# Performance work log

Measured on AMD Instinct MI355X. Metric: run time of the kernel, lower is better.

Reference implementation:

```python
import jax, jax.numpy as jnp
import numpy as np
import itertools

B, T, C, H = 2, 2048, 1024, 8
HD = C // H  # head_dim = 128


def _head_dirs():
    # 8 trigrams = vertices of cube {-1,+1}^3, L2-normalized (norm sqrt(3))
    signs = [-1.0, 1.0]
    tri = np.array(list(itertools.product(signs, repeat=3)), dtype=np.float32)
    tri = tri / np.linalg.norm(tri, axis=1, keepdims=True)
    return jnp.asarray(tri[:H])  # [H, 3]


def setup_inputs() -> dict:
    key = jax.random.key(0)
    ks = jax.random.split(key, 5)
    w = lambda k, sh: jax.random.normal(k, sh, dtype=jnp.float32) * 0.02
    return {
        "x": jax.random.normal(ks[0], (B, T, C), dtype=jnp.float32),
        "Wq": w(ks[1], (H * 3, C)),
        "Wk": w(ks[2], (H * 3, C)),
        "Wv": w(ks[3], (C, C)),
        "Wo": w(ks[4], (C, C)),
        "scale": jnp.asarray(1.0 / np.sqrt(3.0), dtype=jnp.float32),
    }


def reference(x, Wq, Wk, Wv, Wo, scale):
    Bb, Tt, Cc = x.shape
    dirs = _head_dirs()  # [H, 3] constant buffer
    # tiny 3-dim per-head Q/K projections
    q3 = (x @ Wq.T).reshape(Bb, Tt, H, 3).transpose(0, 2, 1, 3)  # [B,H,T,3]
    k3 = (x @ Wk.T).reshape(Bb, Tt, H, 3).transpose(0, 2, 1, 3)  # [B,H,T,3]
    v = (x @ Wv.T).reshape(Bb, Tt, H, HD).transpose(0, 2, 1, 3)  # [B,H,T,HD]
    # projections of q/k onto each head's trigram direction
    q_on_dir = jnp.einsum('bhtd,hd->bht', q3, dirs)  # [B,H,T]
    k_on_dir = jnp.einsum('bhtd,hd->bht', k3, dirs)  # [B,H,T]
    # scores = scaled 3-dim dot product + geometric outer-product bias
    scores = jnp.einsum('bhtd,bhsd->bhts', q3, k3) * scale \
        + q_on_dir[..., :, None] * k_on_dir[..., None, :]  # [B,H,T,T]
    causal = jnp.tril(jnp.ones((Tt, Tt), dtype=bool))
    scores = jnp.where(causal, scores, -jnp.inf)
    attn = jax.nn.softmax(scores, axis=-1)
    out = jnp.einsum('bhts,bhsd->bhtd', attn, v)  # [B,H,T,HD]
    out = out.transpose(0, 2, 1, 3).reshape(Bb, Tt, Cc)
    return out @ Wo.T
```

## Files before the change

kernel.cpp:

```cpp
#include <hip/hip_runtime.h>
#include <hip/hip_bf16.h>

#define B_  2
#define T_  2048
#define C_  1024
#define H_  8
#define HD_ 128
#define M_  (B_*T_)

typedef short  bf16x8 __attribute__((ext_vector_type(8)));
typedef float  f32x4  __attribute__((ext_vector_type(4)));
typedef unsigned short u16x8 __attribute__((ext_vector_type(8)));

typedef const __attribute__((address_space(1))) void* gas_ptr;
typedef __attribute__((address_space(3))) void*       las_ptr;

#define L2E_ 1.4426950408889634f

static __device__ __forceinline__ unsigned short f2bf(float f) {
    unsigned int u = __float_as_uint(f);
    u += 0x7fffu + ((u >> 16) & 1u);
    return (unsigned short)(u >> 16);
}
static __device__ __forceinline__ float bf2f(unsigned short u) {
    return __uint_as_float(((unsigned int)u) << 16);
}
static __device__ __forceinline__ float exp2_fast(float x) {
#if __has_builtin(__builtin_amdgcn_exp2f)
    return __builtin_amdgcn_exp2f(x);
#else
    return exp2f(x);
#endif
}

__global__ __launch_bounds__(256) void k_convert_w(const float* __restrict__ Wv,
                                                   const float* __restrict__ Wo,
                                                   unsigned short* __restrict__ wvbf,
                                                   unsigned short* __restrict__ wobf) {
    int i = blockIdx.x * 256 + threadIdx.x;
    const float* src; unsigned short* dst; int off;
    if (i < 262144) { src = Wv; dst = wvbf; off = i; }
    else            { src = Wo; dst = wobf; off = i - 262144; }
    float4 v = reinterpret_cast<const float4*>(src)[off];
    ushort4 o;
    o.x = f2bf(v.x); o.y = f2bf(v.y); o.z = f2bf(v.z); o.w = f2bf(v.w);
    reinterpret_cast<ushort4*>(dst)[off] = o;
}

__global__ __launch_bounds__(256) void k_proj_qk(const float* __restrict__ x,
                                                 const float* __restrict__ Wq,
                                                 const float* __restrict__ Wk,
                                                 const float* __restrict__ scale_p,
                                                 float* __restrict__ qt,
                                                 float* __restrict__ kt,
                                                 unsigned short* __restrict__ xbf) {
    __shared__ __align__(16) float wl[48][260];
    __shared__ __align__(16) float xl[16][260];
    __shared__ float res[16][48];
    const int tid  = threadIdx.x;
    const int row0 = blockIdx.x << 4;
    const int r    = tid >> 4, sub = tid & 15;
    float a0 = 0.f, a1 = 0.f, a2 = 0.f;

    for (int ch = 0; ch < 4; ++ch) {
        const int k0 = ch * 256;
        #pragma unroll
        for (int i = 0; i < 12; ++i) {
            int fi = i * 256 + tid;
            int wr = fi >> 6, wc = (fi & 63) * 4;
            const float* src = (wr < 24) ? (Wq + (size_t)wr * C_) : (Wk + (size_t)(wr - 24) * C_);
            *reinterpret_cast<float4*>(&wl[wr][wc]) = *reinterpret_cast<const float4*>(src + k0 + wc);
        }
        #pragma unroll
        for (int i = 0; i < 4; ++i) {
            int fi = i * 256 + tid;
            int xr = fi >> 6, xc = (fi & 63) * 4;
            size_t goff = (size_t)(row0 + xr) * C_ + k0 + xc;
            float4 xv = *reinterpret_cast<const float4*>(x + goff);
            *reinterpret_cast<float4*>(&xl[xr][xc]) = xv;
            ushort4 o;
            o.x = f2bf(xv.x); o.y = f2bf(xv.y); o.z = f2bf(xv.z); o.w = f2bf(xv.w);
            *reinterpret_cast<ushort4*>(xbf + goff) = o;
        }
        __syncthreads();
        const int oc = sub * 3;
        #pragma unroll 4
        for (int k = 0; k < 256; k += 4) {
            float4 xv = *reinterpret_cast<const float4*>(&xl[r][k]);
            float4 w0 = *reinterpret_cast<const float4*>(&wl[oc + 0][k]);
            float4 w1 = *reinterpret_cast<const float4*>(&wl[oc + 1][k]);
            float4 w2 = *reinterpret_cast<const float4*>(&wl[oc + 2][k]);
            a0 += xv.x * w0.x + xv.y * w0.y + xv.z * w0.z + xv.w * w0.w;
            a1 += xv.x * w1.x + xv.y * w1.y + xv.z * w1.z + xv.w * w1.w;
            a2 += xv.x * w2.x + xv.y * w2.y + xv.z * w2.z + xv.w * w2.w;
        }
        __syncthreads();
    }
    res[r][sub * 3 + 0] = a0;
    res[r][sub * 3 + 1] = a1;
    res[r][sub * 3 + 2] = a2;
    __syncthreads();

    {
        const int rr = tid >> 4, s2 = tid & 15;
        const int isK = s2 >> 3, h = s2 & 7;
        const float r3 = 0.57735026918962576f;
        float d0 = (h & 4) ? r3 : -r3;
        float d1 = (h & 2) ? r3 : -r3;
        float d2 = (h & 1) ? r3 : -r3;
        const float* v3 = &res[rr][isK * 24 + h * 3];
        float a = v3[0], b = v3[1], c = v3[2];
        float ond = a * d0 + b * d1 + c * d2;
        float sc = scale_p[0];
        float4 ov = isK ? make_float4(a, b, c, ond)
                        : make_float4(a * sc * L2E_, b * sc * L2E_, c * sc * L2E_, ond * L2E_);
        float* dst = isK ? kt : qt;
        int grow = row0 + rr;
        int b_ = grow >> 11, t_idx = grow & (T_ - 1);
        reinterpret_cast<float4*>(dst)[(size_t)(b_ * H_ + h) * T_ + t_idx] = ov;
    }
}

template <int MODE>
__global__ __launch_bounds__(256) void k_gemm128x64(const unsigned short* __restrict__ A,
                                                    const unsigned short* __restrict__ Bw,
                                                    void* __restrict__ Cout,
                                                    int Mdim, int Ndim, int Kdim) {
    __shared__ __align__(16) unsigned short lds_a[8][128][8];
    __shared__ __align__(16) unsigned short lds_b[8][64][8];
    const int tid = threadIdx.x;
    const int nbn = Ndim >> 6;
    const int bm = (blockIdx.x / nbn) << 7;
    const int bn = (blockIdx.x % nbn) << 6;
    const int w = tid >> 6, l = tid & 63;
    const int wm = (w >> 1) << 6, wn = (w & 1) << 5;
    const int lh = l & 15, lq = l >> 4;

    f32x4 acc[4][2];
    #pragma unroll
    for (int i = 0; i < 4; ++i)
        #pragma unroll
        for (int j = 0; j < 2; ++j)
            acc[i][j] = (f32x4){0.f, 0.f, 0.f, 0.f};

    for (int k0 = 0; k0 < Kdim; k0 += 64) {
        #pragma unroll
        for (int p = 0; p < 4; ++p) {
            int flat = p * 256 + tid;
            int kq = flat >> 7, row = flat & 127;
            __builtin_amdgcn_global_load_lds((gas_ptr)(A + (size_t)(bm + row) * Kdim + k0 + kq * 8),
                (las_ptr)(&lds_a[0][0][0] + (size_t)flat * 8), 16, 0, 0);
        }
        #pragma unroll
        for (int p = 0; p < 2; ++p) {
            int flat = p * 256 + tid;
            int kq = flat >> 6, row = flat & 63;
            __builtin_amdgcn_global_load_lds((gas_ptr)(Bw + (size_t)(bn + row) * Kdim + k0 + kq * 8),
                (las_ptr)(&lds_b[0][0][0] + (size_t)flat * 8), 16, 0, 0);
        }
        __syncthreads();

        #pragma unroll
        for (int kk = 0; kk < 2; ++kk) {
            bf16x8 af[4], bfr[2];
            #pragma unroll
            for (int f = 0; f < 4; ++f)
                af[f] = *reinterpret_cast<const bf16x8*>(&lds_a[lq + 4 * kk][wm + f * 16 + lh][0]);
            #pragma unroll
            for (int f = 0; f < 2; ++f)
                bfr[f] = *reinterpret_cast<const bf16x8*>(&lds_b[lq + 4 * kk][wn + f * 16 + lh][0]);
            #pragma unroll
            for (int i = 0; i < 4; ++i)
                #pragma unroll
                for (int j = 0; j < 2; ++j)
                    acc[i][j] = __builtin_amdgcn_mfma_f32_16x16x32_bf16(af[i], bfr[j], acc[i][j], 0, 0, 0);
        }
        __syncthreads();
    }

    if constexpr (MODE == 0) {
        float* Cf = (float*)Cout;
        #pragma unroll
        for (int i = 0; i < 4; ++i) {
            int rbase = bm + wm + i * 16 + lq * 4;
            #pragma unroll
            for (int j = 0; j < 2; ++j) {
                int cidx = bn + wn + j * 16 + lh;
                #pragma unroll
                for (int r = 0; r < 4; ++r)
                    Cf[(size_t)(rbase + r) * Ndim + cidx] = acc[i][j][r];
            }
        }
    } else {
        __shared__ unsigned short ldsT[128][72];
        #pragma unroll
        for (int i = 0; i < 4; ++i)
            #pragma unroll
            for (int j = 0; j < 2; ++j)
                #pragma unroll
                for (int r = 0; r < 4; ++r)
                    ldsT[wm + i * 16 + lq * 4 + r][wn + j * 16 + lh] = f2bf(acc[i][j][r]);
        __syncthreads();
        unsigned short* vt_out = (unsigned short*)Cout;
        int c = tid & 63, part = tid >> 6;
        int b = bm >> 11, t0 = bm & (T_ - 1);
        unsigned short* dst = vt_out + ((size_t)b * C_ + bn + c) * T_ + t0 + part * 32;
        #pragma unroll
        for (int jj = 0; jj < 4; ++jj) {
            u16x8 v;
            #pragma unroll
            for (int k = 0; k < 8; ++k) v[k] = ldsT[part * 32 + jj * 8 + k][c];
            *reinterpret_cast<u16x8*>(dst + jj * 8) = v;
        }
    }
}

__global__ __launch_bounds__(256) void k_attn64(
        const float4* __restrict__ qt, const float4* __restrict__ kt,
        const unsigned short* __restrict__ vt,
        unsigned short* __restrict__ mpart,
        float2* __restrict__ mlbuf,
        int nsp, int lg2nsp) {
    __shared__ __align__(16) unsigned short lv[2][8192];
    __shared__ __align__(16) float4 lk[2][64];
    const int tid = threadIdx.x;
    const int w = tid >> 6, l = tid & 63;
    const int lh = l & 15, lg = l >> 4;
    const int bid = blockIdx.x;
    const int qb = 31 - (bid >> (4 + lg2nsp));
    const int sp = (bid >> 4) & (nsp - 1);
    const int bh = bid & 15;
    const int q0 = qb << 6;
    const int qrow = q0 + 4 * lh + w;
    const int nt = qb + 1;

    const float4* qtb = qt + (size_t)bh * T_;
    const float4* ktb = kt + (size_t)bh * T_;
    const unsigned short* vtb = vt + (size_t)bh * HD_ * T_;

    const unsigned short* vsrc[4];
    #pragma unroll
    for (int i = 0; i < 4; ++i) {
        int f = i * 256 + tid;
        vsrc[i] = vtb + (size_t)((((f >> 6) & 7) * 16) + (f & 15)) * T_
                      + ((f >> 9) << 5) + ((f >> 4) & 3) * 8;
    }

#define STAGE(ST, BUF) do {                                                    \
    int s0_ = (ST) << 6;                                                       \
    __builtin_amdgcn_global_load_lds((gas_ptr)(vsrc[0] + s0_),                 \
        (las_ptr)(&lv[BUF][0] + (size_t)(0 * 256 + tid) * 8), 16, 0, 0);       \
    __builtin_amdgcn_global_load_lds((gas_ptr)(vsrc[1] + s0_),                 \
        (las_ptr)(&lv[BUF][0] + (size_t)(1 * 256 + tid) * 8), 16, 0, 0);       \
    __builtin_amdgcn_global_load_lds((gas_ptr)(vsrc[2] + s0_),                 \
        (las_ptr)(&lv[BUF][0] + (size_t)(2 * 256 + tid) * 8), 16, 0, 0);       \
    __builtin_amdgcn_global_load_lds((gas_ptr)(vsrc[3] + s0_),                 \
        (las_ptr)(&lv[BUF][0] + (size_t)(3 * 256 + tid) * 8), 16, 0, 0);       \
    __builtin_amdgcn_global_load_lds((gas_ptr)(ktb + s0_ + l),                 \
        (las_ptr)(&lk[BUF][0]), 16, 0, 0);                                     \
} while (0)

    const float4 q4 = qtb[qrow];
    f32x4 acc[8];
    #pragma unroll
    for (int n = 0; n < 8; ++n) acc[n] = (f32x4){0.f, 0.f, 0.f, 0.f};
    float m = -1e30f, lsum = 0.f;

    if (sp < nt) STAGE(sp, 0);
    __syncthreads();

    int buf = 0;
    for (int st = sp; st < nt; st += nsp) {
        if (st + nsp < nt) STAGE(st + nsp, buf ^ 1);

        const int s0 = st << 6;
        const int c0 = s0 + lg * 8;
        const int c1 = s0 + 32 + lg * 8;

        float p[16];
        float mt = -1e30f;
        #pragma unroll
        for (int jj = 0; jj < 8; ++jj) {
            float4 k4 = lk[buf][lg * 8 + jj];
            float sc = fmaf(q4.x, k4.x, fmaf(q4.y, k4.y, fmaf(q4.z, k4.z, q4.w * k4.w)));
            sc = (c0 + jj > qrow) ? -1e30f : sc;
            p[jj] = sc;
            mt = fmaxf(mt, sc);
        }
        #pragma unroll
        for (int jj = 0; jj < 8; ++jj) {
            float4 k4 = lk[buf][32 + lg * 8 + jj];
            float sc = fmaf(q4.x, k4.x, fmaf(q4.y, k4.y, fmaf(q4.z, k4.z, q4.w * k4.w)));
            sc = (c1 + jj > qrow) ? -1e30f : sc;
            p[8 + jj] = sc;
            mt = fmaxf(mt, sc);
        }
        mt = fmaxf(mt, __shfl_xor(mt, 16));
        mt = fmaxf(mt, __shfl_xor(mt, 32));
        if (__any(mt > m + 8.f)) {
            float mnew = fmaxf(m, mt);
            float corr = exp2_fast(m - mnew);
            m = mnew;
            lsum *= corr;
            float cc0 = __shfl(corr, 4 * lg + 0);
            float cc1 = __shfl(corr, 4 * lg + 1);
            float cc2 = __shfl(corr, 4 * lg + 2);
            float cc3 = __shfl(corr, 4 * lg + 3);
            #pragma unroll
            for (int n = 0; n < 8; ++n) {
                acc[n][0] *= cc0; acc[n][1] *= cc1; acc[n][2] *= cc2; acc[n][3] *= cc3;
            }
        }
        float ps = 0.f;
        #pragma unroll
        for (int jj = 0; jj < 8; ++jj) {
            float e = exp2_fast(p[jj] - m);
            e = (c0 + jj > qrow) ? 0.f : e;
            p[jj] = e;
            ps += e;
        }
        #pragma unroll
        for (int jj = 0; jj < 8; ++jj) {
            float e = exp2_fast(p[8 + jj] - m);
            e = (c1 + jj > qrow) ? 0.f : e;
            p[8 + jj] = e;
            ps += e;
        }
        ps += __shfl_xor(ps, 16);
        ps += __shfl_xor(ps, 32);
        lsum += ps;

        bf16x8 pa0, pa1;
        #pragma unroll
        for (int jj = 0; jj < 8; ++jj) { pa0[jj] = (short)f2bf(p[jj]); pa1[jj] = (short)f2bf(p[8 + jj]); }

        #pragma unroll
        for (int n = 0; n < 8; ++n) {
            bf16x8 vf = *reinterpret_cast<const bf16x8*>(&lv[buf][(size_t)(n * 64 + lg * 16 + lh) * 8]);
            acc[n] = __builtin_amdgcn_mfma_f32_16x16x32_bf16(pa0, vf, acc[n], 0, 0, 0);
        }
        #pragma unroll
        for (int n = 0; n < 8; ++n) {
            bf16x8 vf = *reinterpret_cast<const bf16x8*>(&lv[buf][(size_t)(512 + n * 64 + lg * 16 + lh) * 8]);
            acc[n] = __builtin_amdgcn_mfma_f32_16x16x32_bf16(pa1, vf, acc[n], 0, 0, 0);
        }

        __syncthreads();
        buf ^= 1;
    }
#undef STAGE

    unsigned short* mp = mpart + (size_t)(sp * 16 + bh) * T_ * HD_;
    #pragma unroll
    for (int n = 0; n < 8; ++n) {
        #pragma unroll
        for (int r = 0; r < 4; ++r) {
            int row = q0 + 16 * lg + 4 * r + w;
            mp[(size_t)row * HD_ + n * 16 + lh] = f2bf(acc[n][r]);
        }
    }
    if (lg == 0)
        mlbuf[(size_t)(sp * 16 + bh) * T_ + qrow] = make_float2(m, lsum);
}

__global__ __launch_bounds__(256) void k_combine(const unsigned short* __restrict__ mpart,
                                                 const float2* __restrict__ mlbuf,
                                                 unsigned short* __restrict__ attnbf,
                                                 int nsp) {
    int idx = blockIdx.x * 256 + threadIdx.x;
    int bh = idx >> 16;
    int rem = idx & 65535;
    int t = rem >> 5, d0 = (rem & 31) * 4;
    float mg = -1e30f, den = 0.f;
    float ax = 0.f, ay = 0.f, az = 0.f, aw = 0.f;
    for (int s = 0; s < nsp; ++s) {
        float2 ml = mlbuf[(size_t)(s * 16 + bh) * T_ + t];
        ushort4 a = *reinterpret_cast<const ushort4*>(
            mpart + ((size_t)(s * 16 + bh) * T_ + t) * HD_ + d0);
        float mn = fmaxf(mg, ml.x);
        float cOld = exp2_fast(mg - mn);
        float cNew = exp2_fast(ml.x - mn);
        den = den * cOld + ml.y * cNew;
        ax = ax * cOld + bf2f(a.x) * cNew;
        ay = ay * cOld + bf2f(a.y) * cNew;
        az = az * cOld + bf2f(a.z) * cNew;
        aw = aw * cOld + bf2f(a.w) * cNew;
        mg = mn;
    }
    float inv = 1.f / den;
    int b = bh >> 3, h = bh & 7;
    ushort4 o;
    o.x = f2bf(ax * inv); o.y = f2bf(ay * inv);
    o.z = f2bf(az * inv); o.w = f2bf(aw * inv);
    *reinterpret_cast<ushort4*>(attnbf + ((size_t)(b * T_ + t) * C_ + h * HD_ + d0)) = o;
}

extern "C" void kernel_launch(void* const* d_in, const int* in_sizes, int n_in,
                              void* d_out, int out_size, void* d_ws, size_t ws_size,
                              hipStream_t stream) {
    const float* x     = (const float*)d_in[0];
    const float* Wq    = (const float*)d_in[1];
    const float* Wk    = (const float*)d_in[2];
    const float* Wv    = (const float*)d_in[3];
    const float* Wo    = (const float*)d_in[4];
    const float* scale = (const float*)d_in[5];
    float* out = (float*)d_out;

    const int nsp    = (ws_size >= 46137344) ? 4 : 2;
    const int lg2nsp = (nsp == 4) ? 2 : 1;

    char* ws = (char*)d_ws;
    size_t o = (size_t)nsp * 8388608;
    unsigned short* mpart  = (unsigned short*)(ws);
    unsigned short* xbf    = (unsigned short*)(ws);
    unsigned short* wvbf   = (unsigned short*)(ws + 8388608);
    float*          qt     = (float*)(ws + o);
    float*          kt     = (float*)(ws + o + 524288);
    unsigned short* vt     = (unsigned short*)(ws + o + 1048576);
    unsigned short* attnbf = (unsigned short*)(ws + o + 1048576);
    unsigned short* wobf   = (unsigned short*)(ws + o + 9437184);
    float2*         mlbuf  = (float2*)(ws + o + 11534336);

    k_convert_w<<<2048, 256, 0, stream>>>(Wv, Wo, wvbf, wobf);

    k_proj_qk<<<M_ / 16, 256, 0, stream>>>(x, Wq, Wk, scale, qt, kt, xbf);

    k_gemm128x64<2><<<(M_ / 128) * (C_ / 64), 256, 0, stream>>>(xbf, wvbf, (void*)vt, M_, C_, C_);

    k_attn64<<<32 * nsp * 16, 256, 0, stream>>>(
        reinterpret_cast<const float4*>(qt), reinterpret_cast<const float4*>(kt), vt,
        mpart, mlbuf, nsp, lg2nsp);

    k_combine<<<4096, 256, 0, stream>>>(mpart, mlbuf, attnbf, nsp);

    k_gemm128x64<0><<<(M_ / 128) * (C_ / 64), 256, 0, stream>>>(attnbf, wobf, (void*)out, M_, C_, C_);
}
```

Measured before the change: 134.5 us.

## Pair causal query blocks per workgroup to share K/V tiles

Each attention workgroup now handles two query blocks, a short one (qa) and its mirrored long one (31-qa). The K/V tiles staged into LDS are reused by both, which halves the grid and evens out the causal triangle's work across blocks. Causal masking is applied only on the diagonal tile, and bf16 packing now uses a perm instruction. The cost is doubled accumulator registers (two sets of 8 f32x4), which may lower occupancy, and with nsp>1 the guard `sp < nt` was dropped, so some splits may stage tiles they never use.

```diff
diff --git a/kernel.cpp b/kernel.cpp
--- a/kernel.cpp
+++ b/kernel.cpp
@@ -11,6 +11,7 @@
 typedef short  bf16x8 __attribute__((ext_vector_type(8)));
 typedef float  f32x4  __attribute__((ext_vector_type(4)));
 typedef unsigned short u16x8 __attribute__((ext_vector_type(8)));
+typedef unsigned int   u32x4 __attribute__((ext_vector_type(4)));
 
 typedef const __attribute__((address_space(1))) void* gas_ptr;
 typedef __attribute__((address_space(3))) void*       las_ptr;
@@ -21,6 +22,10 @@
     unsigned int u = __float_as_uint(f);
     u += 0x7fffu + ((u >> 16) & 1u);
     return (unsigned short)(u >> 16);
+}
+static __device__ __forceinline__ unsigned int rne_u32(float f) {
+    unsigned int u = __float_as_uint(f);
+    return u + 0x7fffu + ((u >> 16) & 1u);
 }
 static __device__ __forceinline__ float bf2f(unsigned short u) {
     return __uint_as_float(((unsigned int)u) << 16);
@@ -215,7 +220,7 @@
     }
 }
 
-__global__ __launch_bounds__(256) void k_attn64(
+__global__ __launch_bounds__(256) void k_attn_pair64(
         const float4* __restrict__ qt, const float4* __restrict__ kt,
         const unsigned short* __restrict__ vt,
         unsigned short* __restrict__ mpart,
@@ -227,12 +232,15 @@
     const int w = tid >> 6, l = tid & 63;
     const int lh = l & 15, lg = l >> 4;
     const int bid = blockIdx.x;
-    const int qb = 31 - (bid >> (4 + lg2nsp));
-    const int sp = (bid >> 4) & (nsp - 1);
-    const int bh = bid & 15;
-    const int q0 = qb << 6;
-    const int qrow = q0 + 4 * lh + w;
-    const int nt = qb + 1;
+    const int pr  = bid >> (4 + lg2nsp);
+    const int sp  = (bid >> 4) & (nsp - 1);
+    const int bh  = bid & 15;
+    const int qa  = pr;
+    const int qbg = 31 - pr;
+    const int q0a = qa << 6, q0b = qbg << 6;
+    const int qrowA = q0a + 4 * lh + w;
+    const int qrowB = q0b + 4 * lh + w;
+    const int nt = qbg + 1;
 
     const float4* qtb = qt + (size_t)bh * T_;
     const float4* ktb = kt + (size_t)bh * T_;
@@ -260,13 +268,105 @@
         (las_ptr)(&lk[BUF][0]), 16, 0, 0);                                     \
 } while (0)
 
-    const float4 q4 = qtb[qrow];
-    f32x4 acc[8];
+#define TILE_GROUP(Q4, MM, LS, ACC, EDGE, QROW) do {                           \
+    float p[16];                                                               \
+    if (!(EDGE)) {                                                             \
+        _Pragma("unroll")                                                      \
+        for (int jj = 0; jj < 8; ++jj) {                                       \
+            float4 k4 = lk[buf][lg * 8 + jj];                                  \
+            p[jj] = fmaf((Q4).x, k4.x, fmaf((Q4).y, k4.y,                      \
+                     fmaf((Q4).z, k4.z, (Q4).w * k4.w)));                      \
+        }                                                                      \
+        _Pragma("unroll")                                                      \
+        for (int jj = 0; jj < 8; ++jj) {                                       \
+            float4 k4 = lk[buf][32 + lg * 8 + jj];                             \
+            p[8 + jj] = fmaf((Q4).x, k4.x, fmaf((Q4).y, k4.y,                  \
+                         fmaf((Q4).z, k4.z, (Q4).w * k4.w)));                  \
+        }                                                                      \
+    } else {                                                                   \
+        _Pragma("unroll")                                                      \
+        for (int jj = 0; jj < 8; ++jj) {                                       \
+            float4 k4 = lk[buf][lg * 8 + jj];                                  \
+            float sc = fmaf((Q4).x, k4.x, fmaf((Q4).y, k4.y,                   \
+                        fmaf((Q4).z, k4.z, (Q4).w * k4.w)));                   \
+            p[jj] = (c0 + jj > (QROW)) ? -1e30f : sc;                          \
+        }                                                                      \
+        _Pragma("unroll")                                                      \
+        for (int jj = 0; jj < 8; ++jj) {                                       \
+            float4 k4 = lk[buf][32 + lg * 8 + jj];                             \
+            float sc = fmaf((Q4).x, k4.x, fmaf((Q4).y, k4.y,                   \
+                        fmaf((Q4).z, k4.z, (Q4).w * k4.w)));                   \
+            p[8 + jj] = (c1 + jj > (QROW)) ? -1e30f : sc;                      \
+        }                                                                      \
+    }                                                                          \
+    float ma = fmaxf(fmaxf(p[0], p[1]), p[2]);                                 \
+    float mb = fmaxf(fmaxf(p[3], p[4]), p[5]);                                 \
+    float mc = fmaxf(fmaxf(p[6], p[7]), p[8]);                                 \
+    float md = fmaxf(fmaxf(p[9], p[10]), p[11]);                               \
+    float me = fmaxf(fmaxf(p[12], p[13]), p[14]);                              \
+    float mt = fmaxf(fmaxf(fmaxf(ma, mb), fmaxf(mc, md)), fmaxf(me, p[15]));   \
+    mt = fmaxf(mt, __shfl_xor(mt, 16));                                        \
+    mt = fmaxf(mt, __shfl_xor(mt, 32));                                        \
+    if (__any(mt > (MM) + 8.f)) {                                              \
+        float mnew = fmaxf((MM), mt);                                          \
+        float corr = exp2_fast((MM) - mnew);                                   \
+        (MM) = mnew;                                                           \
+        (LS) *= corr;                                                          \
+        float cc0 = __shfl(corr, 4 * lg + 0);                                  \
+        float cc1 = __shfl(corr, 4 * lg + 1);                                  \
+        float cc2 = __shfl(corr, 4 * lg + 2);                                  \
+        float cc3 = __shfl(corr, 4 * lg + 3);                                  \
+        _Pragma("unroll")                                                      \
+        for (int n = 0; n < 8; ++n) {                                          \
+            (ACC)[n][0] *= cc0; (ACC)[n][1] *= cc1;                            \
+            (ACC)[n][2] *= cc2; (ACC)[n][3] *= cc3;                            \
+        }                                                                      \
+    }                                                                          \
+    _Pragma("unroll")                                                          \
+    for (int jj = 0; jj < 16; ++jj)                                            \
+        p[jj] = exp2_fast(p[jj] - (MM));                                       \
+    float sa = (p[0] + p[1] + p[2]) + (p[3] + p[4] + p[5]);                    \
+    float sb = (p[6] + p[7] + p[8]) + (p[9] + p[10] + p[11]);                  \
+    float ps = sa + sb + ((p[12] + p[13] + p[14]) + p[15]);                    \
+    ps += __shfl_xor(ps, 16);                                                  \
+    ps += __shfl_xor(ps, 32);                                                  \
+    (LS) += ps;                                                                \
+    u32x4 w0_, w1_;                                                            \
+    _Pragma("unroll")                                                          \
+    for (int i = 0; i < 4; ++i) {                                              \
+        w0_[i] = __builtin_amdgcn_perm(rne_u32(p[2 * i + 1]),                  \
+                                       rne_u32(p[2 * i]), 0x07060302u);        \
+        w1_[i] = __builtin_amdgcn_perm(rne_u32(p[8 + 2 * i + 1]),              \
+                                       rne_u32(p[8 + 2 * i]), 0x07060302u);    \
+    }                                                                          \
+    bf16x8 pa0 = __builtin_bit_cast(bf16x8, w0_);                              \
+    bf16x8 pa1 = __builtin_bit_cast(bf16x8, w1_);                              \
+    _Pragma("unroll")                                                          \
+    for (int n = 0; n < 8; ++n) {                                              \
+        bf16x8 vf = *reinterpret_cast<const bf16x8*>(                          \
+            &lv[buf][(size_t)(n * 64 + lg * 16 + lh) * 8]);                    \
+        (ACC)[n] = __builtin_amdgcn_mfma_f32_16x16x32_bf16(pa0, vf, (ACC)[n], 0, 0, 0); \
+    }                                                                          \
+    _Pragma("unroll")                                                          \
+    for (int n = 0; n < 8; ++n) {                                              \
+        bf16x8 vf = *reinterpret_cast<const bf16x8*>(                          \
+            &lv[buf][(size_t)(512 + n * 64 + lg * 16 + lh) * 8]);              \
+        (ACC)[n] = __builtin_amdgcn_mfma_f32_16x16x32_bf16(pa1, vf, (ACC)[n], 0, 0, 0); \
+    }                                                                          \
+} while (0)
+
+    const float4 q4a = qtb[qrowA];
+    const float4 q4b = qtb[qrowB];
+    f32x4 accA[8], accB[8];
     #pragma unroll
-    for (int n = 0; n < 8; ++n) acc[n] = (f32x4){0.f, 0.f, 0.f, 0.f};
-    float m = -1e30f, lsum = 0.f;
-
-    if (sp < nt) STAGE(sp, 0);
+    for (int n = 0; n < 8; ++n) {
+        accA[n] = (f32x4){0.f, 0.f, 0.f, 0.f};
+        accB[n] = (f32x4){0.f, 0.f, 0.f, 0.f};
+    }
+    float mA = -1e30f, lsA = 0.f;
+    float mB = -1e30f, lsB = 0.f;
+
+    STAGE(sp, 0);
     __syncthreads();
 
     int buf = 0;
@@ -277,77 +377,14 @@
         const int c0 = s0 + lg * 8;
         const int c1 = s0 + 32 + lg * 8;
 
-        float p[16];
-        float mt = -1e30f;
-        #pragma unroll
-        for (int jj = 0; jj < 8; ++jj) {
-            float4 k4 = lk[buf][lg * 8 + jj];
-            float sc = fmaf(q4.x, k4.x, fmaf(q4.y, k4.y, fmaf(q4.z, k4.z, q4.w * k4.w)));
-            sc = (c0 + jj > qrow) ? -1e30f : sc;
-            p[jj] = sc;
-            mt = fmaxf(mt, sc);
-        }
-        #pragma unroll
-        for (int jj = 0; jj < 8; ++jj) {
-            float4 k4 = lk[buf][32 + lg * 8 + jj];
-            float sc = fmaf(q4.x, k4.x, fmaf(q4.y, k4.y, fmaf(q4.z, k4.z, q4.w * k4.w)));
-            sc = (c1 + jj > qrow) ? -1e30f : sc;
-            p[8 + jj] = sc;
-            mt = fmaxf(mt, sc);
-        }
-        mt = fmaxf(mt, __shfl_xor(mt, 16));
-        mt = fmaxf(mt, __shfl_xor(mt, 32));
-        if (__any(mt > m + 8.f)) {
-            float mnew = fmaxf(m, mt);
-            float corr = exp2_fast(m - mnew);
-            m = mnew;
-            lsum *= corr;
-            float cc0 = __shfl(corr, 4 * lg + 0);
-            float cc1 = __shfl(corr, 4 * lg + 1);
-            float cc2 = __shfl(corr, 4 * lg + 2);
-            float cc3 = __shfl(corr, 4 * lg + 3);
-            #pragma unroll
-            for (int n = 0; n < 8; ++n) {
-                acc[n][0] *= cc0; acc[n][1] *= cc1; acc[n][2] *= cc2; acc[n][3] *= cc3;
-            }
-        }
-        float ps = 0.f;
-        #pragma unroll
-        for (int jj = 0; jj < 8; ++jj) {
-            float e = exp2_fast(p[jj] - m);
-            e = (c0 + jj > qrow) ? 0.f : e;
-            p[jj] = e;
-            ps += e;
-        }
-        #pragma unroll
-        for (int jj = 0; jj < 8; ++jj) {
-            float e = exp2_fast(p[8 + jj] - m);
-            e = (c1 + jj > qrow) ? 0.f : e;
-            p[8 + jj] = e;
-            ps += e;
-        }
-        ps += __shfl_xor(ps, 16);
-        ps += __shfl_xor(ps, 32);
-        lsum += ps;
-
-        bf16x8 pa0, pa1;
-        #pragma unroll
-        for (int jj = 0; jj < 8; ++jj) { pa0[jj] = (short)f2bf(p[jj]); pa1[jj] = (short)f2bf(p[8 + jj]); }
-
-        #pragma unroll
-        for (int n = 0; n < 8; ++n) {
-            bf16x8 vf = *reinterpret_cast<const bf16x8*>(&lv[buf][(size_t)(n * 64 + lg * 16 + lh) * 8]);
-            acc[n] = __builtin_amdgcn_mfma_f32_16x16x32_bf16(pa0, vf, acc[n], 0, 0, 0);
-        }
-        #pragma unroll
-        for (int n = 0; n < 8; ++n) {
-            bf16x8 vf = *reinterpret_cast<const bf16x8*>(&lv[buf][(size_t)(512 + n * 64 + lg * 16 + lh) * 8]);
-            acc[n] = __builtin_amdgcn_mfma_f32_16x16x32_bf16(pa1, vf, acc[n], 0, 0, 0);
-        }
+        TILE_GROUP(q4b, mB, lsB, accB, st == qbg, qrowB);
+        if (st <= qa)
+            TILE_GROUP(q4a, mA, lsA, accA, st == qa, qrowA);
 
         __syncthreads();
         buf ^= 1;
     }
+#undef TILE_GROUP
 #undef STAGE
 
     unsigned short* mp = mpart + (size_t)(sp * 16 + bh) * T_ * HD_;
@@ -355,12 +392,16 @@
     for (int n = 0; n < 8; ++n) {
         #pragma unroll
         for (int r = 0; r < 4; ++r) {
-            int row = q0 + 16 * lg + 4 * r + w;
-            mp[(size_t)row * HD_ + n * 16 + lh] = f2bf(acc[n][r]);
-        }
-    }
-    if (lg == 0)
-        mlbuf[(size_t)(sp * 16 + bh) * T_ + qrow] = make_float2(m, lsum);
+            int rowB = q0b + 16 * lg + 4 * r + w;
+            mp[(size_t)rowB * HD_ + n * 16 + lh] = f2bf(accB[n][r]);
+            int rowA = q0a + 16 * lg + 4 * r + w;
+            mp[(size_t)rowA * HD_ + n * 16 + lh] = f2bf(accA[n][r]);
+        }
+    }
+    if (lg == 0) {
+        mlbuf[(size_t)(sp * 16 + bh) * T_ + qrowB] = make_float2(mB, lsB);
+        mlbuf[(size_t)(sp * 16 + bh) * T_ + qrowA] = make_float2(mA, lsA);
+    }
 }
 
 __global__ __launch_bounds__(256) void k_combine(const unsigned short* __restrict__ mpart,
@@ -427,7 +468,7 @@
 
     k_gemm128x64<2><<<(M_ / 128) * (C_ / 64), 256, 0, stream>>>(xbf, wvbf, (void*)vt, M_, C_, C_);
 
-    k_attn64<<<32 * nsp * 16, 256, 0, stream>>>(
+    k_attn_pair64<<<16 * nsp * 16, 256, 0, stream>>>(
         reinterpret_cast<const float4*>(qt), reinterpret_cast<const float4*>(kt), vt,
         mpart, mlbuf, nsp, lg2nsp);
 
```

After: 138.6 us. 3.0% more time.
